# Optimization experiments

Measured on AMD Instinct MI355X. Metric: run time of the kernel, lower is better.

Reference implementation:

```python
import jax, jax.numpy as jnp
import numpy as np

NHEAD = 12
EPS_Z = 1e-5
EPS_LN = 1e-5


def _zscore_last(t, n):
    # torch .std is unbiased (ddof=1)
    m = t.mean(axis=-1, keepdims=True)
    var = ((t - m) ** 2).sum(axis=-1, keepdims=True) / (n - 1)
    return (t - m) / (jnp.sqrt(var) + EPS_Z)


def _layernorm(x, g, b):
    m = x.mean(axis=-1, keepdims=True)
    v = ((x - m) ** 2).mean(axis=-1, keepdims=True)
    return (x - m) * jax.lax.rsqrt(v + EPS_LN) * g + b


def setup_inputs() -> dict:
    key = jax.random.key(0)
    ks = jax.random.split(key, 20)
    B, T, D, FF, E = 2, 1024, 768, 3072, 4
    p = lambda k, shape: (jax.random.normal(k, shape, jnp.float32) * 0.02)
    return {
        "src": jax.random.normal(ks[0], (B, T, D), jnp.float32),
        "frac": jax.random.uniform(ks[1], (B, T), jnp.float32),
        "Wq": p(ks[2], (D, D)), "bq": jnp.zeros((D,), jnp.float32),
        "Wk": p(ks[3], (D, D)), "bk": jnp.zeros((D,), jnp.float32),
        "Wv": p(ks[4], (D, D)), "bv": jnp.zeros((D,), jnp.float32),
        "Wo": p(ks[5], (D, D)), "bo": jnp.zeros((D,), jnp.float32),
        "gamma": jnp.float32(1.0),
        "ln1_g": jnp.ones((D,), jnp.float32), "ln1_b": jnp.zeros((D,), jnp.float32),
        "ln2_g": jnp.ones((D,), jnp.float32), "ln2_b": jnp.zeros((D,), jnp.float32),
        "Wg": p(ks[6], (E, D)), "bg": jnp.zeros((E,), jnp.float32),
        "W1": p(ks[7], (E, D, FF)), "b1": jnp.zeros((E, FF), jnp.float32),
        "W2": p(ks[8], (E, FF, D)), "b2": jnp.zeros((E, D), jnp.float32),
    }


def reference(src, frac, Wq, bq, Wk, bk, Wv, bv, Wo, bo, gamma,
              ln1_g, ln1_b, ln2_g, ln2_b, Wg, bg, W1, b1, W2, b2):
    B, T, D = src.shape
    H = NHEAD
    hd = D // H
    scale = hd ** -0.5

    # ---- attention (add_frac_bias=False path) ----
    Q = (src @ Wq.T + bq).reshape(B, T, H, hd)
    K = (src @ Wk.T + bk).reshape(B, T, H, hd)
    V = (src @ Wv.T + bv).reshape(B, T, H, hd)
    logits = jnp.einsum('bqhd,bkhd->bhqk', Q, K) * scale
    logits = gamma * _zscore_last(logits, T)
    probs = jax.nn.softmax(logits, axis=-1)
    attn = jnp.einsum('bhqk,bkhd->bqhd', probs, V).reshape(B, T, D)
    attn = attn @ Wo.T + bo

    # ---- residual + norm1 ----
    x = _layernorm(src + attn, ln1_g, ln1_b)

    # ---- MoE top-2 feed-forward ----
    E = Wg.shape[0]
    gate_scores = jax.nn.softmax(x @ Wg.T + bg, axis=-1)          # [B,T,E]
    top2_val, top2_idx = jax.lax.top_k(gate_scores, 2)            # [B,T,2]
    combine = (jax.nn.one_hot(top2_idx, E, dtype=x.dtype)
               * top2_val[..., None]).sum(axis=-2)                # [B,T,E]
    h = jax.nn.relu(jnp.einsum('btd,edf->ebtf', x, W1) + b1[:, None, None, :])
    y = jnp.einsum('ebtf,efd->ebtd', h, W2) + b2[:, None, None, :]
    ff = jnp.einsum('ebtd,bte->btd', y, combine)

    # ---- residual + norm2 ----
    return _layernorm(x + ff, ln2_g, ln2_b)
```

## Files before the change

kernel.cpp:

```cpp
#include <hip/hip_runtime.h>

typedef unsigned short u16;
typedef short bf16x8 __attribute__((ext_vector_type(8)));
typedef float f32x4 __attribute__((ext_vector_type(4)));

#define BB 2
#define TT 1024
#define DD 768
#define HH 12
#define HD 64
#define FFD 3072
#define NE 4
#define NTOK (BB*TT)
#define CROWS 4608
#define SLABZ 3538944L

#define MFMA16(a, b, c) __builtin_amdgcn_mfma_f32_16x16x32_bf16((a), (b), (c), 0, 0, 0)

#define ASYNC16(gsrc, ldst)                                                    \
    __builtin_amdgcn_global_load_lds(                                          \
        (const __attribute__((address_space(1))) void*)(gsrc),                 \
        (__attribute__((address_space(3))) void*)(ldst), 16, 0, 0)

__device__ __forceinline__ float us2f(u16 u) {
    return __uint_as_float(((unsigned int)u) << 16);
}
__device__ __forceinline__ u16 f2us(float f) {
    unsigned int x = __float_as_uint(f);
    x += 0x7fffu + ((x >> 16) & 1u);
    return (u16)(x >> 16);
}

__global__ __launch_bounds__(256) void convert5_kernel(
    const float* __restrict__ src, const float* __restrict__ wq,
    const float* __restrict__ wk, const float* __restrict__ wv,
    const float* __restrict__ wo,
    const float* __restrict__ bq, const float* __restrict__ bk,
    const float* __restrict__ bv,
    u16* __restrict__ src_h, u16* __restrict__ wqkv_h, u16* __restrict__ wo_h,
    float* __restrict__ bqkv)
{
    const int bid = blockIdx.x, tid = threadIdx.x;
    if (bid == 1920) {
        for (int i = tid; i < 3 * DD; i += 256) {
            float v = (i < DD) ? bq[i] : (i < 2 * DD) ? bk[i - DD] : bv[i - 2 * DD];
            bqkv[i] = v;
        }
        return;
    }
    int i = bid * 256 + tid;
    const float* in; u16* out; int off;
    if (i < 196608) { in = src; out = src_h; off = i; }
    else {
        int j = i - 196608; int w = j / 73728; off = j - w * 73728;
        in = (w == 0) ? wq : (w == 1) ? wk : (w == 2) ? wv : wo;
        out = (w < 3) ? wqkv_h + (size_t)w * (DD * DD) : wo_h;
    }
    const float4* p = reinterpret_cast<const float4*>(in) + (size_t)off * 2;
    float4 a = p[0], b = p[1];
    u16 o[8] = {f2us(a.x), f2us(a.y), f2us(a.z), f2us(a.w),
                f2us(b.x), f2us(b.y), f2us(b.z), f2us(b.w)};
    *reinterpret_cast<uint4*>(out + (size_t)off * 8) = *reinterpret_cast<uint4*>(o);
}

__global__ __launch_bounds__(256) void transpose_convert_kernel(
    const float* __restrict__ src, u16* __restrict__ dst,
    int C, int dstStride, long srcZ, long dstZ)
{
    __shared__ float tile[32][33];
    const float* s = src + (size_t)blockIdx.z * srcZ;
    u16* d = dst + (size_t)blockIdx.z * dstZ;
    const int c0 = blockIdx.x * 32, r0 = blockIdx.y * 32;
    const int tid = threadIdx.x;
    {
        const int r = tid >> 3, cs = (tid & 7) * 4;
        float4 v = *reinterpret_cast<const float4*>(&s[(size_t)(r0 + r) * C + c0 + cs]);
        tile[r][cs] = v.x; tile[r][cs + 1] = v.y;
        tile[r][cs + 2] = v.z; tile[r][cs + 3] = v.w;
    }
    __syncthreads();
    {
        const int c = tid >> 3, rs = (tid & 7) * 4;
        u16 o[4] = {f2us(tile[rs][c]), f2us(tile[rs + 1][c]),
                    f2us(tile[rs + 2][c]), f2us(tile[rs + 3][c])};
        *reinterpret_cast<uint2*>(&d[(size_t)(c0 + c) * dstStride + r0 + rs]) =
            *reinterpret_cast<uint2*>(o);
    }
}

__global__ __launch_bounds__(256) void scan_build_kernel(
    const int* __restrict__ epack, int* __restrict__ cnt,
    int* __restrict__ rowtok, int* __restrict__ tok2row)
{
    __shared__ int sc[256][4];
    const int tid = threadIdx.x;
    for (int i = tid; i < CROWS; i += 256) rowtok[i] = 0;
    int ep[8];
    int l0 = 0, l1 = 0, l2 = 0, l3 = 0;
    #pragma unroll
    for (int i = 0; i < 8; i++) {
        const int v = epack[tid * 8 + i];
        ep[i] = v;
        const int a = v & 15, b = (v >> 4) & 15;
        l0 += (a == 0) + (b == 0);
        l1 += (a == 1) + (b == 1);
        l2 += (a == 2) + (b == 2);
        l3 += (a == 3) + (b == 3);
    }
    sc[tid][0] = l0; sc[tid][1] = l1; sc[tid][2] = l2; sc[tid][3] = l3;
    __syncthreads();
    for (int off = 1; off < 256; off <<= 1) {
        int v0 = 0, v1 = 0, v2 = 0, v3 = 0;
        if (tid >= off) {
            v0 = sc[tid - off][0]; v1 = sc[tid - off][1];
            v2 = sc[tid - off][2]; v3 = sc[tid - off][3];
        }
        __syncthreads();
        if (tid >= off) {
            sc[tid][0] += v0; sc[tid][1] += v1;
            sc[tid][2] += v2; sc[tid][3] += v3;
        }
        __syncthreads();
    }
    const int t0 = sc[255][0], t1 = sc[255][1], t2 = sc[255][2], t3 = sc[255][3];
    if (tid == 0) { cnt[0] = t0; cnt[1] = t1; cnt[2] = t2; cnt[3] = t3; }
    const int b1 = (t0 + 127) & ~127;
    const int b2 = b1 + ((t1 + 127) & ~127);
    const int b3 = b2 + ((t2 + 127) & ~127);
    int r0 = sc[tid][0] - l0;
    int r1 = b1 + sc[tid][1] - l1;
    int r2 = b2 + sc[tid][2] - l2;
    int r3 = b3 + sc[tid][3] - l3;
    #pragma unroll
    for (int i = 0; i < 8; i++) {
        const int t = tid * 8 + i;
        const int a = ep[i] & 15, b = (ep[i] >> 4) & 15;
        const int ra = (a == 0) ? r0++ : (a == 1) ? r1++ : (a == 2) ? r2++ : r3++;
        rowtok[ra] = t; tok2row[t * 2] = ra;
        const int rb = (b == 0) ? r0++ : (b == 1) ? r1++ : (b == 2) ? r2++ : r3++;
        rowtok[rb] = t; tok2row[t * 2 + 1] = rb;
    }
}

template<int DB>
__global__ __launch_bounds__(256) void gemm_bt_kernel(
    const u16* __restrict__ A, int lda, long aZ,
    const u16* __restrict__ Bt, int ldb, long bZ,
    int K, int mode, int swz,
    float* __restrict__ outF, u16* __restrict__ outH,
    u16* __restrict__ outH2, u16* __restrict__ outH3,
    int ldc, long cZ,
    const float* __restrict__ biasF, int biasZ,
    const int* __restrict__ rowtok, const int* __restrict__ cntp,
    const float* __restrict__ comb)
{
    __shared__ __align__(16) u16 As[(DB ? 2 : 1) * 128 * 64];
    __shared__ __align__(16) u16 Bs[(DB ? 2 : 1) * 128 * 64];
    const int tid = threadIdx.x;
    int bx, by, z, e = 0, baseE = 0;
    if (swz == 3) {
        const int fid = blockIdx.x;
        const int xcd = fid & 7; int r = fid >> 3;
        const int half = (r >= 96) ? 1 : 0; r -= half * 96;
        bx = r % 6; by = r / 6;
        const int ez = xcd * 2 + half; e = ez >> 2; z = ez & 3;
    } else if (swz == 1) {
        const int fid = blockIdx.x;
        const int xcd = fid & 7; const int r = fid >> 3;
        const int ne = xcd * 12 + (r % 12);
        by = r / 12; bx = ne % 24; e = ne / 24; z = e;
    } else if (swz == 2) {
        const int fid = blockIdx.x;
        const int g = (fid & 7) * 36 + (fid >> 3);
        by = g & 15; bx = g >> 4; z = 0;
    } else {
        bx = blockIdx.x; by = blockIdx.y; z = blockIdx.z;
    }
    if (mode == 2 || mode == 4) {
        const int q0 = (cntp[0] + 127) & ~127;
        const int q1 = (cntp[1] + 127) & ~127;
        const int q2 = (cntp[2] + 127) & ~127;
        baseE = (e > 0 ? q0 : 0) + (e > 1 ? q1 : 0) + (e > 2 ? q2 : 0);
        if (by * 128 >= cntp[e]) return;
    }
    const int m0 = by * 128, n0 = bx * 128;
    const u16* Ab = A + (size_t)z * aZ;
    const u16* Bb = Bt + (size_t)z * bZ;
    if (mode == 4) {
        Ab += (size_t)baseE * lda;
        Bb += (size_t)e * ((size_t)DD * FFD);
    }

    const int wave = tid >> 6, lane = tid & 63;
    const int wm = (wave & 1) * 64, wn = (wave >> 1) * 64;
    const int fm = lane & 15;
    const int g  = lane >> 4;

    const int lr8 = lane >> 3;
    const int cg  = ((lane & 7) ^ lr8) * 8;
    const u16 *aG[4], *bG[4];
    u16 *aL[4], *bL[4];
    #pragma unroll
    for (int i = 0; i < 4; i++) {
        const int rr = wave * 32 + i * 8 + lr8;
        int arow;
        if (mode == 2) arow = rowtok[baseE + m0 + rr];
        else           arow = m0 + rr;
        aG[i] = Ab + (size_t)arow * lda + cg;
        bG[i] = Bb + (size_t)(n0 + rr) * ldb + cg;
        aL[i] = &As[(wave * 32 + i * 8) * 64];
        bL[i] = &Bs[(wave * 32 + i * 8) * 64];
    }

#define STAGE(B, KO) do {                                                      \
        const int _o = (B) * (128 * 64);                                       \
        _Pragma("unroll")                                                      \
        for (int _i = 0; _i < 4; _i++) ASYNC16(aG[_i] + (KO), aL[_i] + _o);    \
        _Pragma("unroll")                                                      \
        for (int _i = 0; _i < 4; _i++) ASYNC16(bG[_i] + (KO), bL[_i] + _o);    \
    } while (0)

    const int c0 = ((g    ) ^ (fm & 7)) * 8;
    const int c1 = ((g + 4) ^ (fm & 7)) * 8;
    const u16* pa[4]; const u16* pb[4];
    #pragma unroll
    for (int i = 0; i < 4; i++) {
        pa[i] = &As[(wm + i * 16 + fm) * 64];
        pb[i] = &Bs[(wn + i * 16 + fm) * 64];
    }

    f32x4 acc[4][4] = {};
    int buf = 0;
    if (DB) STAGE(0, 0);

    for (int k0 = 0; k0 < K; k0 += 64) {
        if (DB) {
            asm volatile("s_waitcnt vmcnt(0)" ::: "memory");
            __builtin_amdgcn_s_barrier();
            __builtin_amdgcn_sched_barrier(0);
            if (k0 + 64 < K) STAGE(buf ^ 1, k0 + 64);
        } else {
            STAGE(0, k0);
            __syncthreads();
        }
        const int bo = DB ? buf * (128 * 64) : 0;
        #pragma unroll
        for (int ks = 0; ks < 2; ks++) {
            const int cc = bo + (ks ? c1 : c0);
            bf16x8 af[4], bf[4];
            #pragma unroll
            for (int i = 0; i < 4; i++)
                af[i] = *reinterpret_cast<const bf16x8*>(pa[i] + cc);
            #pragma unroll
            for (int j = 0; j < 4; j++)
                bf[j] = *reinterpret_cast<const bf16x8*>(pb[j] + cc);
            #pragma unroll
            for (int i = 0; i < 4; i++)
                #pragma unroll
                for (int j = 0; j < 4; j++)
                    acc[i][j] = MFMA16(af[i], bf[j], acc[i][j]);
        }
        if (DB) buf ^= 1;
        else    __syncthreads();
    }
    if (DB) __syncthreads();
#undef STAGE

    const int cn = lane & 15, cr = (lane >> 4) * 4;

    if (mode == 0) {
        const int which = (n0 >= 1536) ? 2 : (n0 >= 768 ? 1 : 0);
        const int nb = n0 - which * 768;
        u16* outP = (which == 0) ? outH : (which == 1) ? outH2 : outH3;
        u16* Cs = As;
        #pragma unroll
        for (int i = 0; i < 4; i++) {
            if (i) __syncthreads();
            #pragma unroll
            for (int j = 0; j < 4; j++) {
                const int n = n0 + wn + j * 16 + cn;
                const float bias = biasF[n];
                #pragma unroll
                for (int r = 0; r < 4; r++) {
                    Cs[((wave & 1) * 16 + cr + r) * 128 + wn + j * 16 + cn] =
                        f2us(acc[i][j][r] + bias);
                }
            }
            __syncthreads();
            if (which < 2) {
                const int lr2 = tid >> 3, c2 = (tid & 7) * 16;
                const int m2 = m0 + (lr2 >> 4) * 64 + i * 16 + (lr2 & 15);
                const int bb2 = m2 >> 10, t2 = m2 & 1023;
                const int hh = (nb + c2) >> 6, d0 = (nb + c2) & 63;
                u16* dst = outP + (((size_t)(bb2 * HH + hh) * TT + t2) << 6) + d0;
                *reinterpret_cast<uint4*>(dst) =
                    *reinterpret_cast<const uint4*>(&Cs[lr2 * 128 + c2]);
                *reinterpret_cast<uint4*>(dst + 8) =
                    *reinterpret_cast<const uint4*>(&Cs[lr2 * 128 + c2 + 8]);
            } else {
                const int nl = tid >> 1, half = tid & 1;
                const int hh = (nb + nl) >> 6, d = (nb + nl) & 63;
                #pragma unroll
                for (int seg = 0; seg < 2; seg++) {
                    u16 o[8];
                    #pragma unroll
                    for (int k = 0; k < 8; k++)
                        o[k] = Cs[(seg * 16 + half * 8 + k) * 128 + nl];
                    const int t0 = m0 + seg * 64 + i * 16 + half * 8;
                    const int bb2 = t0 >> 10, tt2 = t0 & 1023;
                    u16* dst = outP + (((size_t)(bb2 * HH + hh) * HD + d) << 10) + tt2;
                    *reinterpret_cast<uint4*>(dst) = *reinterpret_cast<uint4*>(o);
                }
            }
        }
        return;
    }

    if (mode == 2) {
        u16* Cs = As;
        #pragma unroll
        for (int i = 0; i < 4; i++) {
            if (i) __syncthreads();
            int tokr[4]; float combr[4];
            #pragma unroll
            for (int r = 0; r < 4; r++)
                tokr[r] = rowtok[baseE + m0 + wm + i * 16 + cr + r];
            #pragma unroll
            for (int r = 0; r < 4; r++)
                combr[r] = comb[(size_t)tokr[r] * NE + z];
            #pragma unroll
            for (int j = 0; j < 4; j++) {
                const int n = n0 + wn + j * 16 + cn;
                const float bias = biasF[(size_t)z * biasZ + n];
                #pragma unroll
                for (int r = 0; r < 4; r++) {
                    float y = fmaxf(acc[i][j][r] + bias, 0.f) * combr[r];
                    Cs[((wave & 1) * 16 + cr + r) * 128 + wn + j * 16 + cn] = f2us(y);
                }
            }
            __syncthreads();
            const int lr2 = tid >> 3, c2 = (tid & 7) * 16;
            const int m2 = m0 + (lr2 >> 4) * 64 + i * 16 + (lr2 & 15);
            u16* dst = outH + (size_t)(baseE + m2) * ldc + n0 + c2;
            *reinterpret_cast<uint4*>(dst) =
                *reinterpret_cast<const uint4*>(&Cs[lr2 * 128 + c2]);
            *reinterpret_cast<uint4*>(dst + 8) =
                *reinterpret_cast<const uint4*>(&Cs[lr2 * 128 + c2 + 8]);
        }
        return;
    }

    #pragma unroll
    for (int i = 0; i < 4; i++) {
        #pragma unroll
        for (int j = 0; j < 4; j++) {
            const int n = n0 + wn + j * 16 + cn;
            #pragma unroll
            for (int r = 0; r < 4; r++) {
                const int m = m0 + wm + i * 16 + cr + r;
                float* basep = outF + (size_t)z * cZ;
                basep[(size_t)(baseE + m) * ldc + n] = acc[i][j][r];
            }
        }
    }
}

#define PSTR 1032
__global__ __launch_bounds__(256, 4) void attn_mfma_kernel(
    const u16* __restrict__ Qh, const u16* __restrict__ Kh,
    const u16* __restrict__ VT, const float* __restrict__ gamma_p,
    u16* __restrict__ attn_out)
{
    __shared__ __align__(16) u16 P[16 * PSTR];
    __shared__ float wred[4][16][4];
    __shared__ float dred[4][16];
    __shared__ float aArr[16], cmArr[16], dinvArr[16];

    const int qt = blockIdx.x, bh = blockIdx.y;
    const int b = bh / HH, h = bh - b * HH;
    const int tid = threadIdx.x, wave = tid >> 6, lane = tid & 63;
    const int g = lane >> 4, fm = lane & 15;
    const float gamma = gamma_p[0];
    const int m0 = qt * 16;
    const u16* Qp = Qh + (size_t)bh * TT * HD;
    const u16* Kp = Kh + (size_t)bh * TT * HD;
    const u16* Vp = VT + (size_t)bh * HD * TT;

    bf16x8 af[2];
    #pragma unroll
    for (int ks = 0; ks < 2; ks++)
        af[ks] = *reinterpret_cast<const bf16x8*>(
            Qp + (size_t)(m0 + fm) * HD + ks * 32 + g * 8);

    const int n0w = wave * 256;
    f32x4 acc[16] = {};
    #pragma unroll
    for (int nj = 0; nj < 16; nj++) {
        const u16* kp = Kp + (size_t)(n0w + nj * 16 + fm) * HD + g * 8;
        bf16x8 b0 = *reinterpret_cast<const bf16x8*>(kp);
        bf16x8 b1 = *reinterpret_cast<const bf16x8*>(kp + 32);
        acc[nj] = MFMA16(af[0], b0, acc[nj]);
        acc[nj] = MFMA16(af[1], b1, acc[nj]);
    }

    #pragma unroll
    for (int r = 0; r < 4; r++) {
        float s1 = 0.f, s2 = 0.f, mx = -3.4e38f, mn = 3.4e38f;
        #pragma unroll
        for (int nj = 0; nj < 16; nj++) {
            float v = acc[nj][r];
            s1 += v; s2 = fmaf(v, v, s2);
            mx = fmaxf(mx, v); mn = fminf(mn, v);
        }
        #pragma unroll
        for (int msk = 1; msk < 16; msk <<= 1) {
            s1 += __shfl_xor(s1, msk);
            s2 += __shfl_xor(s2, msk);
            mx = fmaxf(mx, __shfl_xor(mx, msk));
            mn = fminf(mn, __shfl_xor(mn, msk));
        }
        if (fm == 0) {
            int row = g * 4 + r;
            wred[wave][row][0] = s1; wred[wave][row][1] = s2;
            wred[wave][row][2] = mx; wred[wave][row][3] = mn;
        }
    }
    __syncthreads();
    if (tid < 16) {
        float s1 = 0.f, s2 = 0.f, mx = -3.4e38f, mn = 3.4e38f;
        #pragma unroll
        for (int w = 0; w < 4; w++) {
            s1 += wred[w][tid][0]; s2 += wred[w][tid][1];
            mx = fmaxf(mx, wred[w][tid][2]); mn = fminf(mn, wred[w][tid][3]);
        }
        float var = (s2 - s1 * s1 * (1.f / TT)) * (1.f / (TT - 1));
        var = fmaxf(var, 0.f);
        float a = gamma / (sqrtf(var) + 8e-5f);
        aArr[tid] = a;
        cmArr[tid] = (a >= 0.f) ? a * mx : a * mn;
    }
    __syncthreads();

    #pragma unroll
    for (int r = 0; r < 4; r++) {
        const int row = g * 4 + r;
        const float a = aArr[row], cm = cmArr[row];
        float dp = 0.f;
        #pragma unroll
        for (int nj = 0; nj < 16; nj++) {
            float p = __expf(fmaf(a, acc[nj][r], -cm));
            u16 pb = f2us(p);
            dp += us2f(pb);
            P[row * PSTR + n0w + nj * 16 + fm] = pb;
        }
        #pragma unroll
        for (int msk = 1; msk < 16; msk <<= 1) dp += __shfl_xor(dp, msk);
        if (fm == 0) dred[wave][row] = dp;
    }
    __syncthreads();
    if (tid < 16)
        dinvArr[tid] = 1.f / (dred[0][tid] + dred[1][tid] + dred[2][tid] + dred[3][tid]);
    __syncthreads();

    f32x4 oacc = {};
    #pragma unroll 4
    for (int ks = 0; ks < 32; ks++) {
        bf16x8 bv = *reinterpret_cast<const bf16x8*>(
            Vp + (size_t)(wave * 16 + fm) * TT + ks * 32 + g * 8);
        bf16x8 a0 = *reinterpret_cast<const bf16x8*>(&P[(size_t)fm * PSTR + ks * 32 + g * 8]);
        oacc = MFMA16(a0, bv, oacc);
    }
    #pragma unroll
    for (int r = 0; r < 4; r++) {
        int row = g * 4 + r;
        int t = m0 + row;
        attn_out[((size_t)(b * TT + t)) * DD + h * HD + wave * 16 + fm] =
            f2us(oacc[r] * dinvArr[row]);
    }
}

__global__ __launch_bounds__(256) void ln1_kernel(
    const float* __restrict__ p0, const float* __restrict__ p1,
    const float* __restrict__ p2, const float* __restrict__ p3,
    const float* __restrict__ src, const float* __restrict__ bo,
    const float* __restrict__ g, const float* __restrict__ bta,
    const float* __restrict__ Wg, const float* __restrict__ bg,
    float* __restrict__ outF, u16* __restrict__ outH,
    float* __restrict__ comb, int* __restrict__ epack)
{
    const int row = blockIdx.x, tid = threadIdx.x;
    __shared__ float red[256];
    __shared__ float gred[4][4];
    const size_t base = (size_t)row * DD;
    float v[3];
    #pragma unroll
    for (int i = 0; i < 3; i++) {
        int c = tid + i * 256;
        v[i] = p0[base + c] + p1[base + c] + p2[base + c] + p3[base + c]
             + src[base + c] + bo[c];
    }
    float s = v[0] + v[1] + v[2];
    red[tid] = s; __syncthreads();
    #pragma unroll
    for (int o = 128; o > 0; o >>= 1) { if (tid < o) red[tid] += red[tid + o]; __syncthreads(); }
    const float mean = red[0] * (1.f / 768.f);
    __syncthreads();
    float qv = 0.f;
    #pragma unroll
    for (int i = 0; i < 3; i++) { float d = v[i] - mean; qv += d * d; }
    red[tid] = qv; __syncthreads();
    #pragma unroll
    for (int o = 128; o > 0; o >>= 1) { if (tid < o) red[tid] += red[tid + o]; __syncthreads(); }
    const float var = red[0] * (1.f / 768.f);
    const float rs = rsqrtf(var + 1e-5f);
    float ga0 = 0.f, ga1 = 0.f, ga2 = 0.f, ga3 = 0.f;
    #pragma unroll
    for (int i = 0; i < 3; i++) {
        int c = tid + i * 256;
        float o = (v[i] - mean) * rs * g[c] + bta[c];
        outF[base + c] = o;
        outH[base + c] = f2us(o);
        ga0 = fmaf(o, Wg[c], ga0);
        ga1 = fmaf(o, Wg[DD + c], ga1);
        ga2 = fmaf(o, Wg[2 * DD + c], ga2);
        ga3 = fmaf(o, Wg[3 * DD + c], ga3);
    }
    #pragma unroll
    for (int off = 32; off > 0; off >>= 1) {
        ga0 += __shfl_down(ga0, off, 64);
        ga1 += __shfl_down(ga1, off, 64);
        ga2 += __shfl_down(ga2, off, 64);
        ga3 += __shfl_down(ga3, off, 64);
    }
    const int wave = tid >> 6, lane = tid & 63;
    if (lane == 0) {
        gred[wave][0] = ga0; gred[wave][1] = ga1;
        gred[wave][2] = ga2; gred[wave][3] = ga3;
    }
    __syncthreads();
    if (tid == 0) {
        float gg[NE];
        #pragma unroll
        for (int e = 0; e < NE; e++)
            gg[e] = gred[0][e] + gred[1][e] + gred[2][e] + gred[3][e] + bg[e];
        float m = -1e30f;
        #pragma unroll
        for (int e = 0; e < NE; e++) m = fmaxf(m, gg[e]);
        float ex[NE], ssum = 0.f;
        #pragma unroll
        for (int e = 0; e < NE; e++) { ex[e] = __expf(gg[e] - m); ssum += ex[e]; }
        #pragma unroll
        for (int e = 0; e < NE; e++) ex[e] /= ssum;
        int e1 = 0;
        #pragma unroll
        for (int e = 1; e < NE; e++) if (ex[e] > ex[e1]) e1 = e;
        int e2 = -1;
        #pragma unroll
        for (int e = 0; e < NE; e++) if (e != e1 && (e2 < 0 || ex[e] > ex[e2])) e2 = e;
        float c[NE] = {0.f, 0.f, 0.f, 0.f};
        c[e1] = ex[e1]; c[e2] = ex[e2];
        #pragma unroll
        for (int e = 0; e < NE; e++) comb[(size_t)row * NE + e] = c[e];
        epack[row] = e1 | (e2 << 4);
    }
}

__global__ __launch_bounds__(256) void ln2_kernel(
    const float* __restrict__ x, const float* __restrict__ pslab,
    const int* __restrict__ tok2row,
    const float* __restrict__ comb, const float* __restrict__ b2,
    const float* __restrict__ g, const float* __restrict__ bta,
    float* __restrict__ outF)
{
    const int row = blockIdx.x, tid = threadIdx.x;
    __shared__ float red[256];
    const size_t base = (size_t)row * DD;
    const int r0 = tok2row[row * 2], r1 = tok2row[row * 2 + 1];
    const float* q0 = pslab + (size_t)r0 * DD;
    const float* q1 = pslab + (size_t)r1 * DD;
    const float c0 = comb[row * NE + 0], c1 = comb[row * NE + 1];
    const float c2 = comb[row * NE + 2], c3 = comb[row * NE + 3];
    float v[3];
    #pragma unroll
    for (int i = 0; i < 3; i++) {
        int c = tid + i * 256;
        float t = x[base + c];
        t += q0[c] + q0[SLABZ + c] + q0[2 * SLABZ + c] + q0[3 * SLABZ + c];
        t += q1[c] + q1[SLABZ + c] + q1[2 * SLABZ + c] + q1[3 * SLABZ + c];
        t = fmaf(c0, b2[c], t);
        t = fmaf(c1, b2[DD + c], t);
        t = fmaf(c2, b2[2 * DD + c], t);
        t = fmaf(c3, b2[3 * DD + c], t);
        v[i] = t;
    }
    float s = v[0] + v[1] + v[2];
    red[tid] = s; __syncthreads();
    #pragma unroll
    for (int o = 128; o > 0; o >>= 1) { if (tid < o) red[tid] += red[tid + o]; __syncthreads(); }
    const float mean = red[0] * (1.f / 768.f);
    __syncthreads();
    float qv = 0.f;
    #pragma unroll
    for (int i = 0; i < 3; i++) { float d = v[i] - mean; qv += d * d; }
    red[tid] = qv; __syncthreads();
    #pragma unroll
    for (int o = 128; o > 0; o >>= 1) { if (tid < o) red[tid] += red[tid + o]; __syncthreads(); }
    const float var = red[0] * (1.f / 768.f);
    const float rs = rsqrtf(var + 1e-5f);
    #pragma unroll
    for (int i = 0; i < 3; i++) {
        int c = tid + i * 256;
        outF[base + c] = (v[i] - mean) * rs * g[c] + bta[c];
    }
}

extern "C" void kernel_launch(void* const* d_in, const int* in_sizes, int n_in,
                              void* d_out, int out_size, void* d_ws, size_t ws_size,
                              hipStream_t stream)
{
    const float* src  = (const float*)d_in[0];
    const float* Wq   = (const float*)d_in[2];  const float* bq = (const float*)d_in[3];
    const float* Wk   = (const float*)d_in[4];  const float* bk = (const float*)d_in[5];
    const float* Wv   = (const float*)d_in[6];  const float* bv = (const float*)d_in[7];
    const float* Wo   = (const float*)d_in[8];  const float* bo = (const float*)d_in[9];
    const float* gam  = (const float*)d_in[10];
    const float* ln1g = (const float*)d_in[11]; const float* ln1b = (const float*)d_in[12];
    const float* ln2g = (const float*)d_in[13]; const float* ln2b = (const float*)d_in[14];
    const float* Wg   = (const float*)d_in[15]; const float* bg = (const float*)d_in[16];
    const float* W1   = (const float*)d_in[17]; const float* b1 = (const float*)d_in[18];
    const float* W2   = (const float*)d_in[19]; const float* b2 = (const float*)d_in[20];
    (void)ws_size; (void)in_sizes; (void)n_in; (void)out_size;

    char* ws = (char*)d_ws;
    u16*   W1T  = (u16*)(ws);
    float* wop  = (float*)(ws + 18874368);
    float* pslab= (float*)(ws);
    u16*   W2T  = (u16*)(ws + 56623104);
    u16*   hb   = (u16*)(ws + 75497472);
    float* x    = (float*)(ws + 103809024);
    u16*   xh   = (u16*)(ws + 110100480);
    float* comb = (float*)(ws + 113246208);
    float* bqkv = (float*)(ws + 113278976);
    int*   cnt    = (int*)(ws + 113288192);
    int*   rowtok = (int*)(ws + 113288256);
    int*   epack  = (int*)(ws + 113306688);
    int*   tok2row= (int*)(ws + 113323072);
    char* H = ws + 75497472;
    u16*   Qh     = (u16*)(H);
    u16*   Kh     = (u16*)(H + 3145728);
    u16*   VTh    = (u16*)(H + 6291456);
    u16*   src_h  = (u16*)(H + 9437184);
    u16*   attn_h = (u16*)(H + 12582912);
    u16*   WqkvH  = (u16*)(H + 15728640);
    u16*   WoH    = (u16*)(H + 19267584);
    const long PZ = (long)NTOK * DD;

    convert5_kernel<<<1921, 256, 0, stream>>>(
        src, Wq, Wk, Wv, Wo, bq, bk, bv, src_h, WqkvH, WoH, bqkv);
    transpose_convert_kernel<<<dim3(FFD / 32, DD / 32, NE), 256, 0, stream>>>(
        W1, W1T, FFD, DD, (long)DD * FFD, (long)FFD * DD);
    transpose_convert_kernel<<<dim3(DD / 32, FFD / 32, NE), 256, 0, stream>>>(
        W2, W2T, DD, FFD, (long)FFD * DD, (long)FFD * DD);

    gemm_bt_kernel<1><<<dim3(288, 1, 1), 256, 0, stream>>>(
        src_h, DD, 0, WqkvH, DD, 0, DD, 0, 2,
        nullptr, Qh, Kh, VTh, 0, 0, bqkv, 0, nullptr, nullptr, nullptr);

    attn_mfma_kernel<<<dim3(TT / 16, BB * HH), 256, 0, stream>>>(
        Qh, Kh, VTh, gam, attn_h);

    gemm_bt_kernel<1><<<dim3(DD / 128, NTOK / 128, 4), 256, 0, stream>>>(
        attn_h, DD, 192L, WoH, DD, 192L, 192, 3, 0,
        wop, nullptr, nullptr, nullptr, DD, PZ, nullptr, 0, nullptr, nullptr, nullptr);

    ln1_kernel<<<NTOK, 256, 0, stream>>>(
        wop, wop + PZ, wop + 2 * PZ, wop + 3 * PZ, src, bo,
        ln1g, ln1b, Wg, bg, x, xh, comb, epack);

    scan_build_kernel<<<1, 256, 0, stream>>>(epack, cnt, rowtok, tok2row);

    gemm_bt_kernel<0><<<dim3(1536, 1, 1), 256, 0, stream>>>(
        xh, DD, 0, W1T, DD, (long)FFD * DD, DD, 2, 1,
        nullptr, hb, nullptr, nullptr, FFD, 0, b1, FFD, rowtok, cnt, comb);

    gemm_bt_kernel<0><<<dim3(1536, 1, 1), 256, 0, stream>>>(
        hb, FFD, 768L, W2T, FFD, 768L, 768, 4, 3,
        pslab, nullptr, nullptr, nullptr, DD, SLABZ, nullptr, 0, rowtok, cnt, nullptr);

    ln2_kernel<<<NTOK, 256, 0, stream>>>(
        x, pslab, tok2row, comb, b2, ln2g, ln2b, (float*)d_out);
}
```

Before: 354.1 us.

## Double-buffer K/V register loads and drop extra barriers in attention kernel

The attention kernel now loads K fragments in groups with register double-buffering and raises wave priority around the MFMA bursts. The first V group is prefetched before the softmax statistics, and later V groups are double-buffered the same way. Per-row scale and denominator reductions are now computed redundantly by every thread from float4 LDS reads, which removes two __syncthreads and the single-thread reduction steps. Register pressure rises, which could reduce occupancy under launch_bounds(256,4).

Result: slower. 361.8 us (+2.2%).

```diff
diff --git a/kernel.cpp b/kernel.cpp
--- a/kernel.cpp
+++ b/kernel.cpp
@@ -372,9 +372,8 @@
     u16* __restrict__ attn_out)
 {
     __shared__ __align__(16) u16 P[16 * PSTR];
-    __shared__ float wred[4][16][4];
-    __shared__ float dred[4][16];
-    __shared__ float aArr[16], cmArr[16], dinvArr[16];
+    __shared__ __align__(16) float wred[4][16][4];
+    __shared__ __align__(16) float dred[16][4];
 
     const int qt = blockIdx.x, bh = blockIdx.y;
     const int b = bh / HH, h = bh - b * HH;
@@ -393,15 +392,45 @@
             Qp + (size_t)(m0 + fm) * HD + ks * 32 + g * 8);
 
     const int n0w = wave * 256;
+
     f32x4 acc[16] = {};
-    #pragma unroll
-    for (int nj = 0; nj < 16; nj++) {
-        const u16* kp = Kp + (size_t)(n0w + nj * 16 + fm) * HD + g * 8;
-        bf16x8 b0 = *reinterpret_cast<const bf16x8*>(kp);
-        bf16x8 b1 = *reinterpret_cast<const bf16x8*>(kp + 32);
-        acc[nj] = MFMA16(af[0], b0, acc[nj]);
-        acc[nj] = MFMA16(af[1], b1, acc[nj]);
-    }
+    bf16x8 kr[2][4];
+#define KLOAD(BUF, GRP) do {                                                   \
+        _Pragma("unroll")                                                      \
+        for (int _j = 0; _j < 2; _j++) {                                       \
+            const u16* _kp = Kp +                                              \
+                (size_t)(n0w + ((GRP) * 2 + _j) * 16 + fm) * HD + g * 8;       \
+            kr[BUF][2 * _j]     = *reinterpret_cast<const bf16x8*>(_kp);       \
+            kr[BUF][2 * _j + 1] = *reinterpret_cast<const bf16x8*>(_kp + 32);  \
+        } } while (0)
+    KLOAD(0, 0);
+    #pragma unroll
+    for (int grp = 0; grp < 8; grp++) {
+        const int cur = grp & 1;
+        if (grp < 7) {
+            if (cur == 0) KLOAD(1, grp + 1);
+            else          KLOAD(0, grp + 1);
+        }
+        __builtin_amdgcn_s_setprio(1);
+        #pragma unroll
+        for (int j = 0; j < 2; j++) {
+            const int nj = grp * 2 + j;
+            acc[nj] = MFMA16(af[0], kr[cur][2 * j],     acc[nj]);
+            acc[nj] = MFMA16(af[1], kr[cur][2 * j + 1], acc[nj]);
+        }
+        __builtin_amdgcn_s_setprio(0);
+    }
+#undef KLOAD
+
+    bf16x8 vr[2][4];
+#define VLOAD(BUF, GRP) do {                                                   \
+        _Pragma("unroll")                                                      \
+        for (int _j = 0; _j < 4; _j++) {                                       \
+            const int _ks = (GRP) * 4 + _j;                                    \
+            vr[BUF][_j] = *reinterpret_cast<const bf16x8*>(                    \
+                Vp + (size_t)(wave * 16 + fm) * TT + _ks * 32 + g * 8);        \
+        } } while (0)
+    VLOAD(0, 0);
 
     #pragma unroll
     for (int r = 0; r < 4; r++) {
@@ -420,31 +449,35 @@
             mn = fminf(mn, __shfl_xor(mn, msk));
         }
         if (fm == 0) {
-            int row = g * 4 + r;
+            const int row = g * 4 + r;
             wred[wave][row][0] = s1; wred[wave][row][1] = s2;
             wred[wave][row][2] = mx; wred[wave][row][3] = mn;
         }
     }
     __syncthreads();
-    if (tid < 16) {
+
+    float aR[4], cmR[4];
+    #pragma unroll
+    for (int r = 0; r < 4; r++) {
+        const int row = g * 4 + r;
         float s1 = 0.f, s2 = 0.f, mx = -3.4e38f, mn = 3.4e38f;
         #pragma unroll
         for (int w = 0; w < 4; w++) {
-            s1 += wred[w][tid][0]; s2 += wred[w][tid][1];
-            mx = fmaxf(mx, wred[w][tid][2]); mn = fminf(mn, wred[w][tid][3]);
+            float4 t = *reinterpret_cast<const float4*>(&wred[w][row][0]);
+            s1 += t.x; s2 += t.y;
+            mx = fmaxf(mx, t.z); mn = fminf(mn, t.w);
         }
         float var = (s2 - s1 * s1 * (1.f / TT)) * (1.f / (TT - 1));
         var = fmaxf(var, 0.f);
-        float a = gamma / (sqrtf(var) + 8e-5f);
-        aArr[tid] = a;
-        cmArr[tid] = (a >= 0.f) ? a * mx : a * mn;
-    }
-    __syncthreads();
+        const float a = gamma / (sqrtf(var) + 8e-5f);
+        aR[r] = a;
+        cmR[r] = (a >= 0.f) ? a * mx : a * mn;
+    }
 
     #pragma unroll
     for (int r = 0; r < 4; r++) {
         const int row = g * 4 + r;
-        const float a = aArr[row], cm = cmArr[row];
+        const float a = aR[r], cm = cmR[r];
         float dp = 0.f;
         #pragma unroll
         for (int nj = 0; nj < 16; nj++) {
@@ -455,27 +488,38 @@
         }
         #pragma unroll
         for (int msk = 1; msk < 16; msk <<= 1) dp += __shfl_xor(dp, msk);
-        if (fm == 0) dred[wave][row] = dp;
+        if (fm == 0) dred[row][wave] = dp;
     }
     __syncthreads();
-    if (tid < 16)
-        dinvArr[tid] = 1.f / (dred[0][tid] + dred[1][tid] + dred[2][tid] + dred[3][tid]);
-    __syncthreads();
 
     f32x4 oacc = {};
-    #pragma unroll 4
-    for (int ks = 0; ks < 32; ks++) {
-        bf16x8 bv = *reinterpret_cast<const bf16x8*>(
-            Vp + (size_t)(wave * 16 + fm) * TT + ks * 32 + g * 8);
-        bf16x8 a0 = *reinterpret_cast<const bf16x8*>(&P[(size_t)fm * PSTR + ks * 32 + g * 8]);
-        oacc = MFMA16(a0, bv, oacc);
-    }
+    #pragma unroll
+    for (int grp = 0; grp < 8; grp++) {
+        const int cur = grp & 1;
+        if (grp < 7) {
+            if (cur == 0) VLOAD(1, grp + 1);
+            else          VLOAD(0, grp + 1);
+        }
+        __builtin_amdgcn_s_setprio(1);
+        #pragma unroll
+        for (int j = 0; j < 4; j++) {
+            const int ks = grp * 4 + j;
+            bf16x8 a0 = *reinterpret_cast<const bf16x8*>(
+                &P[(size_t)fm * PSTR + ks * 32 + g * 8]);
+            oacc = MFMA16(a0, vr[cur][j], oacc);
+        }
+        __builtin_amdgcn_s_setprio(0);
+    }
+#undef VLOAD
+
     #pragma unroll
     for (int r = 0; r < 4; r++) {
-        int row = g * 4 + r;
-        int t = m0 + row;
+        const int row = g * 4 + r;
+        float4 dv = *reinterpret_cast<const float4*>(&dred[row][0]);
+        const float dinv = 1.f / (dv.x + dv.y + dv.z + dv.w);
+        const int t = m0 + row;
         attn_out[((size_t)(b * TT + t)) * DD + h * HD + wave * 16 + fm] =
-            f2us(oacc[r] * dinvArr[row]);
+            f2us(oacc[r] * dinv);
     }
 }
 
```
